# Performance work log

Measured on AMD Instinct MI355X. Metric: run time of the kernel, lower is better.

Reference implementation:

```python
import math
import jax
import jax.numpy as jnp
import numpy as np

N_IMG = 8
A = 3
H = 100
W = 100
STRIDE = 16
IMG = 1600
PRE_NMS_TOP_N = 2000
POST_NMS_TOP_N = 1000
NMS_THRESH = 0.7
MIN_SIZE = 0
BBOX_XFORM_CLIP = math.log(1000.0 / 16.0)


def setup_inputs() -> dict:
    key = jax.random.key(0)
    k1, k2 = jax.random.split(key)
    objectness = jax.random.normal(k1, (N_IMG, A, H, W), jnp.float32)
    box_regression = jax.random.normal(k2, (N_IMG, A * 4, H, W), jnp.float32) * 0.5
    # Grid anchors, flattened in (H, W, A) order to match objectness.permute(0,2,3,1)
    cy = (jnp.arange(H, dtype=jnp.float32) + 0.5) * STRIDE  # [H]
    cx = (jnp.arange(W, dtype=jnp.float32) + 0.5) * STRIDE  # [W]
    half = jnp.array([64.0, 128.0, 256.0], jnp.float32) / 2.0  # [A]
    cy = cy[:, None, None]  # [H,1,1]
    cx = cx[None, :, None]  # [1,W,1]
    s = half[None, None, :]  # [1,1,A]
    x1, y1, x2, y2 = jnp.broadcast_arrays(cx - s, cy - s, cx + s, cy + s)
    anc = jnp.stack([x1, y1, x2, y2], axis=-1).reshape(-1, 4)  # [H*W*A, 4]
    anchors = jnp.broadcast_to(anc[None], (N_IMG, H * W * A, 4)).copy()
    return {
        "objectness": objectness,
        "box_regression": box_regression,
        "anchors": anchors,
        "image_height": IMG,
        "image_width": IMG,
    }


def _decode(deltas, boxes):
    # BoxCoder(weights=(1,1,1,1)).decode with TO_REMOVE=1
    widths = boxes[..., 2] - boxes[..., 0] + 1.0
    heights = boxes[..., 3] - boxes[..., 1] + 1.0
    ctr_x = boxes[..., 0] + 0.5 * widths
    ctr_y = boxes[..., 1] + 0.5 * heights
    dx, dy = deltas[..., 0], deltas[..., 1]
    dw = jnp.minimum(deltas[..., 2], BBOX_XFORM_CLIP)
    dh = jnp.minimum(deltas[..., 3], BBOX_XFORM_CLIP)
    pcx = dx * widths + ctr_x
    pcy = dy * heights + ctr_y
    pw = jnp.exp(dw) * widths
    ph = jnp.exp(dh) * heights
    return jnp.stack(
        [pcx - 0.5 * pw, pcy - 0.5 * ph, pcx + 0.5 * pw - 1.0, pcy + 0.5 * ph - 1.0],
        axis=-1,
    )


def _nms_keep(boxes, valid, thresh):
    # boxes [n,4] sorted by descending score; valid: pre-filter mask.
    n = boxes.shape[0]
    x1, y1, x2, y2 = boxes[:, 0], boxes[:, 1], boxes[:, 2], boxes[:, 3]
    areas = (x2 - x1 + 1.0) * (y2 - y1 + 1.0)
    xx1 = jnp.maximum(x1[:, None], x1[None, :])
    yy1 = jnp.maximum(y1[:, None], y1[None, :])
    xx2 = jnp.minimum(x2[:, None], x2[None, :])
    yy2 = jnp.minimum(y2[:, None], y2[None, :])
    inter = jnp.maximum(xx2 - xx1 + 1.0, 0.0) * jnp.maximum(yy2 - yy1 + 1.0, 0.0)
    iou = inter / (areas[:, None] + areas[None, :] - inter)
    idx = jnp.arange(n)

    def body(i, keep):
        sup = keep[i] & (iou[i] > thresh) & (idx > i)
        return keep & ~sup

    return jax.lax.fori_loop(0, n, body, valid)


def _forward(objectness, box_regression, anchors, image_height, image_width):
    N, A_, H_, W_ = objectness.shape
    scores = jax.nn.sigmoid(objectness.transpose(0, 2, 3, 1).reshape(N, -1))  # [N, A*H*W]
    deltas = (
        box_regression.reshape(N, A_, 4, H_, W_)
        .transpose(0, 3, 4, 1, 2)
        .reshape(N, -1, 4)
    )
    pre = min(PRE_NMS_TOP_N, scores.shape[1])
    top_scores, top_idx = jax.lax.top_k(scores, pre)  # sorted descending
    deltas = jnp.take_along_axis(deltas, top_idx[:, :, None], axis=1)
    anc = jnp.take_along_axis(anchors, top_idx[:, :, None], axis=1)
    props = _decode(deltas, anc)  # [N, pre, 4]
    # clip to image (fact = 1)
    xs = jnp.clip(props[..., 0::2], 0.0, image_width - 1.0)
    ys = jnp.clip(props[..., 1::2], 0.0, image_height - 1.0)
    props = jnp.stack([xs[..., 0], ys[..., 0], xs[..., 1], ys[..., 1]], axis=-1)
    # filter small / out-of-image-center boxes
    ws = props[..., 2] - props[..., 0] + 1.0
    hs = props[..., 3] - props[..., 1] + 1.0
    xc = props[..., 0] + ws / 2.0
    yc = props[..., 1] + hs / 2.0
    valid = (ws >= MIN_SIZE) & (hs >= MIN_SIZE) & (xc < image_width) & (yc < image_height)
    keep = jax.vmap(lambda b, v: _nms_keep(b, v, NMS_THRESH))(props, valid)

    def _select(b, s, k):
        # compact kept boxes (already score-sorted) into fixed-size output
        rank = jnp.cumsum(k) - 1
        tgt = jnp.where(k & (rank < POST_NMS_TOP_N), rank, POST_NMS_TOP_N)
        ob = jnp.zeros((POST_NMS_TOP_N + 1, 4), b.dtype).at[tgt].set(b)[:POST_NMS_TOP_N]
        os = jnp.zeros((POST_NMS_TOP_N + 1,), s.dtype).at[tgt].set(s)[:POST_NMS_TOP_N]
        ov = jnp.arange(POST_NMS_TOP_N) < jnp.minimum(jnp.sum(k), POST_NMS_TOP_N)
        return ob, os, ov

    return jax.vmap(_select)(props, top_scores, keep)


def reference(objectness, box_regression, anchors, image_height, image_width):
    # Returns (boxes [N,post,4], objectness scores [N,post], valid mask [N,post])
    return _forward(objectness, box_regression, anchors, image_height, image_width)
```

## Files before the change

kernel.cpp:

```cpp
#include <hip/hip_runtime.h>
#include <math.h>
#include <stdint.h>

#define NIMG   8
#define NA     30000
#define PRE_N  2000
#define POST_N 1000
#define NMS_TH 0.7f
#define DCLIP  4.135166556742356f
#define IMGF   1600.0f
#define IMGM1  1599.0f
#define CAND_MAX 4096


__global__ __launch_bounds__(1024) void hist_compact(
    const float* __restrict__ obj,
    uint64_t* __restrict__ candBuf, unsigned int* __restrict__ candCnt)
{
    const int n    = blockIdx.x;
    const int tid  = threadIdx.x;
    const int lane = tid & 63;
    const int wid  = tid >> 6;

    __shared__ unsigned int hist[4096];
    __shared__ unsigned int wsum[16];
    __shared__ unsigned int scal[4];

    for (int b = tid; b < 4096; b += 1024) hist[b] = 0u;
    if (tid < 4) scal[tid] = 0u;
    __syncthreads();

    const float* objn = obj + n * NA;

    for (int j = tid; j < NA; j += 1024) {
        unsigned int u = __float_as_uint(objn[j]);
        unsigned int k = (u & 0x80000000u) ? ~u : (u | 0x80000000u);
        atomicAdd(&hist[k >> 20], 1u);
    }
    __syncthreads();

    unsigned int c0 = hist[tid*4+0], c1 = hist[tid*4+1],
                 c2 = hist[tid*4+2], c3 = hist[tid*4+3];
    unsigned int p = c0 + c1 + c2 + c3;
    unsigned int s = p;
    #pragma unroll
    for (int off = 1; off < 64; off <<= 1) {
        unsigned int v = __shfl_down(s, off);
        if (lane + off < 64) s += v;
    }
    if (lane == 0) wsum[wid] = s;
    __syncthreads();
    unsigned int wafter = 0;
    for (int w = wid + 1; w < 16; ++w) wafter += wsum[w];
    unsigned int after = (s - p) + wafter;
    {
        unsigned int S3 = after + c3;
        unsigned int S2 = S3 + c2;
        unsigned int S1 = S2 + c1;
        unsigned int S0 = S1 + c0;
        if (S3 >= PRE_N && after < PRE_N) { scal[2] = tid*4+3; }
        if (S2 >= PRE_N && S3    < PRE_N) { scal[2] = tid*4+2; }
        if (S1 >= PRE_N && S2    < PRE_N) { scal[2] = tid*4+1; }
        if (S0 >= PRE_N && S1    < PRE_N) { scal[2] = tid*4+0; }
    }
    __syncthreads();
    const unsigned int bstar = scal[2];

    for (int j = tid; j < NA; j += 1024) {
        unsigned int u = __float_as_uint(objn[j]);
        unsigned int k = (u & 0x80000000u) ? ~u : (u | 0x80000000u);
        if ((k >> 20) < bstar) continue;
        int a = j / 10000, t = j - a * 10000;
        uint64_t key = (((uint64_t)(~k)) << 32) | (unsigned int)(t * 3 + a);
        unsigned int pos = atomicAdd(&scal[0], 1u);
        if (pos < CAND_MAX) candBuf[n * CAND_MAX + pos] = key;
    }
    __syncthreads();
    if (tid == 0) candCnt[n] = min(scal[0], (unsigned int)CAND_MAX);
}

__global__ __launch_bounds__(64) void rank_decode(
    const float* __restrict__ breg,
    const uint64_t* __restrict__ candBuf, const unsigned int* __restrict__ candCnt,
    float* __restrict__ wsBoxes, float* __restrict__ wsScores,
    int* __restrict__ wsValid)
{
    const int n    = blockIdx.x >> 6;
    const int tile = blockIdx.x & 63;
    const int lane = threadIdx.x;

    const int C = (int)candCnt[n];
    if (tile * 64 >= C) return;

    const uint64_t* cb = candBuf + n * CAND_MAX;
    const int my = tile * 64 + lane;
    const uint64_t km = (my < C) ? cb[my] : ~0ull;

    unsigned int rank = 0;
    const int nch = (C + 63) >> 6;
    for (int ch = 0; ch < nch; ++ch) {
        const int j = ch * 64 + lane;
        uint64_t ck = (j < C) ? cb[j] : ~0ull;
        unsigned int clo = (unsigned int)ck, chi = (unsigned int)(ck >> 32);
        #pragma unroll
        for (int c = 0; c < 64; ++c) {
            unsigned int lo = (unsigned int)__builtin_amdgcn_readlane((int)clo, c);
            unsigned int hi = (unsigned int)__builtin_amdgcn_readlane((int)chi, c);
            uint64_t kc = ((uint64_t)hi << 32) | lo;
            rank += (kc < km) ? 1u : 0u;
        }
    }
    if (my >= C || rank >= PRE_N) return;

    unsigned int idx = (unsigned int)km;
    unsigned int k   = ~((unsigned int)(km >> 32));
    unsigned int u   = (k & 0x80000000u) ? (k & 0x7fffffffu) : ~k;
    float logit = __uint_as_float(u);
    float score = 1.0f / (1.0f + expf(-logit));

    int a = idx % 3, t = idx / 3, w = t % 100, h = t / 100;
    const float* bp = breg + n*120000 + (a*4)*10000 + t;
    float dx = bp[0], dy = bp[10000], dw = bp[20000], dh = bp[30000];

    float half = (a == 0) ? 32.0f : ((a == 1) ? 64.0f : 128.0f);
    float cx = w * 16.0f + 8.0f, cy = h * 16.0f + 8.0f;
    float x1 = cx - half, y1 = cy - half, x2 = cx + half, y2 = cy + half;
    float wd = x2 - x1 + 1.0f, hg = y2 - y1 + 1.0f;
    float cxr = x1 + 0.5f * wd, cyr = y1 + 0.5f * hg;
    dw = fminf(dw, DCLIP); dh = fminf(dh, DCLIP);
    float pcx = dx * wd + cxr, pcy = dy * hg + cyr;
    float pw = expf(dw) * wd, ph = expf(dh) * hg;
    float px1 = pcx - 0.5f * pw, py1 = pcy - 0.5f * ph;
    float px2 = pcx + 0.5f * pw - 1.0f, py2 = pcy + 0.5f * ph - 1.0f;
    px1 = fminf(fmaxf(px1, 0.0f), IMGM1);
    px2 = fminf(fmaxf(px2, 0.0f), IMGM1);
    py1 = fminf(fmaxf(py1, 0.0f), IMGM1);
    py2 = fminf(fmaxf(py2, 0.0f), IMGM1);
    float wss = px2 - px1 + 1.0f, hss = py2 - py1 + 1.0f;
    float xc = px1 + wss * 0.5f, yc = py1 + hss * 0.5f;
    int valid = (wss >= 0.0f) && (hss >= 0.0f) && (xc < IMGF) && (yc < IMGF);

    ((float4*)wsBoxes)[n * PRE_N + (int)rank] = make_float4(px1, py1, px2, py2);
    wsScores[n * PRE_N + (int)rank] = score;
    wsValid [n * PRE_N + (int)rank] = valid;
}

__global__ __launch_bounds__(512) void nms_mask(
    const float* __restrict__ wsBoxes, uint64_t* __restrict__ mask)
{
    const int blk  = blockIdx.x;
    const int n    = blk >> 5;
    const int i_t  = blk & 31;
    const int tid  = threadIdx.x;
    const int lane = tid & 63;
    const int wv   = tid >> 6;

    __shared__ uint64_t tile[64 * 33];

    for (int idx = tid; idx < 64 * 33; idx += 512) tile[idx] = 0ull;
    __syncthreads();

    const int r = i_t * 64 + lane;
    float4 rb = (r < PRE_N) ? ((const float4*)wsBoxes)[n * PRE_N + r]
                            : make_float4(0.f, 0.f, 0.f, 0.f);
    float ra = (rb.z - rb.x + 1.0f) * (rb.w - rb.y + 1.0f);

    for (int j_t = i_t + wv; j_t < 32; j_t += 8) {
        const int j = j_t * 64 + lane;
        float4 cb = (j < PRE_N) ? ((const float4*)wsBoxes)[n * PRE_N + j]
                                : make_float4(3e30f, 3e30f, 3e30f, 3e30f);
        float ca = (cb.z - cb.x + 1.0f) * (cb.w - cb.y + 1.0f);
        const uint64_t jmask = (j_t == 31) ? 0xFFFFull : ~0ull;
        const bool diag = (j_t == i_t);
        uint64_t myword = 0ull;

        #pragma unroll
        for (int c = 0; c < 64; ++c) {
            float rx1 = __int_as_float(__builtin_amdgcn_readlane(__float_as_int(rb.x), c));
            float ry1 = __int_as_float(__builtin_amdgcn_readlane(__float_as_int(rb.y), c));
            float rx2 = __int_as_float(__builtin_amdgcn_readlane(__float_as_int(rb.z), c));
            float ry2 = __int_as_float(__builtin_amdgcn_readlane(__float_as_int(rb.w), c));
            float rar = __int_as_float(__builtin_amdgcn_readlane(__float_as_int(ra), c));
            float xx1 = fmaxf(rx1, cb.x), yy1 = fmaxf(ry1, cb.y);
            float xx2 = fminf(rx2, cb.z), yy2 = fminf(ry2, cb.w);
            float ww = fmaxf(xx2 - xx1 + 1.0f, 0.0f);
            float hh = fmaxf(yy2 - yy1 + 1.0f, 0.0f);
            float inter = ww * hh;
            float denom = rar + ca - inter;
            unsigned long long bits = __ballot(inter > NMS_TH * denom) & jmask;
            if (diag) bits &= (c == 63) ? 0ull : ((~0ull) << (c + 1));
            if (lane == c) myword = bits;
        }
        tile[lane * 33 + j_t] = myword;
    }
    __syncthreads();

    uint64_t* mrow = mask + ((size_t)n * PRE_N + (size_t)i_t * 64) * 32;
    const int cmax = (i_t == 31) ? 16 : 64;
    for (int idx = tid; idx < cmax * 32; idx += 512) {
        const int rr = idx >> 5, w = idx & 31;
        mrow[idx] = tile[rr * 33 + w];
    }
}

#define SL(n,b) \
    "global_load_dword v" #n ", %[voff], %[sbase]\n\t" \
    "v_add_u32 %[voff], 0x100, %[voff]\n\t"

#define SS(n,b) \
    "s_waitcnt vmcnt(63)\n\t" \
    "v_readlane_b32 %[t], v" #n ", %[lw]\n\t" \
    "s_bitcmp1_b32 %[win], " #b "\n\t" \
    "s_cselect_b32 %[m], 0, -1\n\t" \
    "s_sub_i32 %[kept], %[kept], %[m]\n\t" \
    "s_and_b32 %[t], %[t], %[m]\n\t" \
    "s_or_b32 %[win], %[win], %[t]\n\t" \
    "v_and_b32 v" #n ", %[m], v" #n "\n\t" \
    "v_or_b32 %[rem], %[rem], v" #n "\n\t" \
    "global_load_dword v" #n ", %[voff], %[sbase]\n\t" \
    "v_add_u32 %[voff], 0x100, %[voff]\n\t"

#define SN(n,b,w) \
    "s_waitcnt vmcnt(" #w ")\n\t" \
    "v_readlane_b32 %[t], v" #n ", %[lw]\n\t" \
    "s_bitcmp1_b32 %[win], " #b "\n\t" \
    "s_cselect_b32 %[m], 0, -1\n\t" \
    "s_sub_i32 %[kept], %[kept], %[m]\n\t" \
    "s_and_b32 %[t], %[t], %[m]\n\t" \
    "s_or_b32 %[win], %[win], %[t]\n\t" \
    "v_and_b32 v" #n ", %[m], v" #n "\n\t" \
    "v_or_b32 %[rem], %[rem], v" #n "\n\t"

#define SWIN \
    "s_add_u32 %[lw], %[lw], 1\n\t" \
    "v_readlane_b32 %[t], %[rem], %[lw]\n\t" \
    "s_mov_b32 %[win], %[t]\n\t"

#define ROW_A(M) M(64,0) M(65,1) M(66,2) M(67,3) M(68,4) M(69,5) M(70,6) M(71,7) \
    M(72,8) M(73,9) M(74,10) M(75,11) M(76,12) M(77,13) M(78,14) M(79,15) \
    M(80,16) M(81,17) M(82,18) M(83,19) M(84,20) M(85,21) M(86,22) M(87,23) \
    M(88,24) M(89,25) M(90,26) M(91,27) M(92,28) M(93,29) M(94,30) M(95,31)
#define ROW_B(M) M(96,0) M(97,1) M(98,2) M(99,3) M(100,4) M(101,5) M(102,6) M(103,7) \
    M(104,8) M(105,9) M(106,10) M(107,11) M(108,12) M(109,13) M(110,14) M(111,15) \
    M(112,16) M(113,17) M(114,18) M(115,19) M(116,20) M(117,21) M(118,22) M(119,23) \
    M(120,24) M(121,25) M(122,26) M(123,27) M(124,28) M(125,29) M(126,30) M(127,31)

__global__ __launch_bounds__(256) void nms_scan_select(
    const float* __restrict__ wsBoxes, const float* __restrict__ wsScores,
    const int* __restrict__ wsValid, const uint64_t* __restrict__ mask,
    float* __restrict__ out)
{
    const int n   = blockIdx.x;
    const int tid = threadIdx.x;

    __shared__ __align__(8) unsigned char invb[256];
    __shared__ unsigned int keepw32[64];
    __shared__ int sscan[256];

    unsigned int byte = 0xFFu;
    if (tid < PRE_N / 8) {
        byte = 0u;
        for (int q = 0; q < 8; ++q)
            byte |= (wsValid[n * PRE_N + tid * 8 + q] ? 0u : 1u) << q;
    }
    invb[tid] = (unsigned char)byte;
    __syncthreads();

    if (tid < 64) {
        unsigned int rem = ((const unsigned int*)invb)[tid];
        unsigned long long sbase =
            (unsigned long long)(const void*)(mask + (size_t)n * PRE_N * 32);
        unsigned int voff = (unsigned int)(tid * 4);
        int win_, m_, t_, lw_, kept_, cnt_;

        asm volatile(
            "s_waitcnt vmcnt(0) lgkmcnt(0)\n\t"
            "s_mov_b32 %[kept], 0\n\t"
            "s_mov_b32 %[lw], 0\n\t"
            ROW_A(SL) ROW_B(SL)
            "v_readlane_b32 %[t], %[rem], %[lw]\n\t"
            "s_mov_b32 %[win], %[t]\n\t"
            "s_mov_b32 %[cnt], 30\n\t"
            "Lnms_%=:\n\t"
            ROW_A(SS)
            SWIN
            ROW_B(SS)
            SWIN
            "s_cmp_ge_i32 %[kept], 0x3e8\n\t"
            "s_cbranch_scc1 Lend_%=\n\t"
            "s_sub_u32 %[cnt], %[cnt], 1\n\t"
            "s_cmp_lg_u32 %[cnt], 0\n\t"
            "s_cbranch_scc1 Lnms_%=\n\t"
            SS(64,0) SS(65,1) SS(66,2) SS(67,3) SS(68,4) SS(69,5) SS(70,6) SS(71,7)
            SS(72,8) SS(73,9) SS(74,10) SS(75,11) SS(76,12) SS(77,13) SS(78,14) SS(79,15)
            SN(80,16,63) SN(81,17,62) SN(82,18,61) SN(83,19,60)
            SN(84,20,59) SN(85,21,58) SN(86,22,57) SN(87,23,56)
            SN(88,24,55) SN(89,25,54) SN(90,26,53) SN(91,27,52)
            SN(92,28,51) SN(93,29,50) SN(94,30,49) SN(95,31,48)
            SWIN
            SN(96,0,47) SN(97,1,46) SN(98,2,45) SN(99,3,44)
            SN(100,4,43) SN(101,5,42) SN(102,6,41) SN(103,7,40)
            SN(104,8,39) SN(105,9,38) SN(106,10,37) SN(107,11,36)
            SN(108,12,35) SN(109,13,34) SN(110,14,33) SN(111,15,32)
            SN(112,16,31) SN(113,17,30) SN(114,18,29) SN(115,19,28)
            SN(116,20,27) SN(117,21,26) SN(118,22,25) SN(119,23,24)
            SN(120,24,23) SN(121,25,22) SN(122,26,21) SN(123,27,20)
            SN(124,28,19) SN(125,29,18) SN(126,30,17) SN(127,31,16)
            SWIN
            SN(64,0,15) SN(65,1,14) SN(66,2,13) SN(67,3,12)
            SN(68,4,11) SN(69,5,10) SN(70,6,9) SN(71,7,8)
            SN(72,8,7) SN(73,9,6) SN(74,10,5) SN(75,11,4)
            SN(76,12,3) SN(77,13,2) SN(78,14,1) SN(79,15,0)
            "Lend_%=:\n\t"
            "s_waitcnt vmcnt(0)\n\t"
            : [rem]"+v"(rem), [voff]"+v"(voff),
              [win]"=&s"(win_), [m]"=&s"(m_), [t]"=&s"(t_),
              [lw]"=&s"(lw_), [kept]"=&s"(kept_), [cnt]"=&s"(cnt_)
            : [sbase]"s"(sbase)
            : "scc", "vcc", "memory",
              "v64","v65","v66","v67","v68","v69","v70","v71",
              "v72","v73","v74","v75","v76","v77","v78","v79",
              "v80","v81","v82","v83","v84","v85","v86","v87",
              "v88","v89","v90","v91","v92","v93","v94","v95",
              "v96","v97","v98","v99","v100","v101","v102","v103",
              "v104","v105","v106","v107","v108","v109","v110","v111",
              "v112","v113","v114","v115","v116","v117","v118","v119",
              "v120","v121","v122","v123","v124","v125","v126","v127");

        keepw32[tid] = ~rem;
    }
    __syncthreads();

    int c[8]; const int base8 = tid * 8;
    int lsum = 0;
    for (int q = 0; q < 8; ++q) {
        const int i = base8 + q;
        c[q] = (i < PRE_N) ? (int)((keepw32[i >> 5] >> (i & 31)) & 1u) : 0;
        lsum += c[q];
    }
    sscan[tid] = lsum;
    __syncthreads();
    for (int off = 1; off < 256; off <<= 1) {
        int v = (tid >= off) ? sscan[tid - off] : 0;
        __syncthreads();
        sscan[tid] += v;
        __syncthreads();
    }
    const int excl  = sscan[tid] - lsum;
    const int total = sscan[255];

    float* ob  = out + n * POST_N * 4;
    float* osc = out + NIMG * POST_N * 4 + n * POST_N;
    float* ovd = out + NIMG * POST_N * 5 + n * POST_N;

    for (int i = tid; i < POST_N * 4; i += 256) ob[i] = 0.0f;
    for (int i = tid; i < POST_N; i += 256) osc[i] = 0.0f;
    const int lim = min(total, POST_N);
    for (int i = tid; i < POST_N; i += 256) ovd[i] = (i < lim) ? 1.0f : 0.0f;
    __syncthreads();

    int run = excl;
    for (int q = 0; q < 8; ++q) {
        const int i = base8 + q;
        if (i < PRE_N && c[q]) {
            if (run < POST_N) {
                float4 b = ((const float4*)wsBoxes)[n * PRE_N + i];
                ob[run * 4 + 0] = b.x;
                ob[run * 4 + 1] = b.y;
                ob[run * 4 + 2] = b.z;
                ob[run * 4 + 3] = b.w;
                osc[run] = wsScores[n * PRE_N + i];
            }
            run++;
        }
    }
}

extern "C" void kernel_launch(void* const* d_in, const int* in_sizes, int n_in,
                              void* d_out, int out_size, void* d_ws, size_t ws_size,
                              hipStream_t stream) {
    const float* obj  = (const float*)d_in[0];
    const float* breg = (const float*)d_in[1];
    float* ws        = (float*)d_ws;
    float* wsBoxes   = ws;
    float* wsScores  = ws + 64000;
    int*   wsValid   = (int*)(ws + 80000);
    uint64_t* wsMask = (uint64_t*)(ws + 96000);
    uint64_t*     candBuf = wsMask;
    unsigned int* candCnt = (unsigned int*)(wsMask + NIMG * CAND_MAX);

    hist_compact<<<NIMG, 1024, 0, stream>>>(obj, candBuf, candCnt);
    rank_decode<<<NIMG * 64, 64, 0, stream>>>(breg, candBuf, candCnt,
                                              wsBoxes, wsScores, wsValid);
    nms_mask<<<NIMG * 32, 512, 0, stream>>>(wsBoxes, wsMask);
    nms_scan_select<<<NIMG, 256, 0, stream>>>(wsBoxes, wsScores, wsValid, wsMask,
                                              (float*)d_out);
}
```

Baseline: 184.1 us.

## Fuse NMS mask and scan kernels via last-block-done atomic counter

New measurement: 190.9 us. 1.04x slower.

```diff
diff --git a/kernel.cpp b/kernel.cpp
--- a/kernel.cpp
+++ b/kernel.cpp
@@ -15,7 +15,8 @@
 
 __global__ __launch_bounds__(1024) void hist_compact(
     const float* __restrict__ obj,
-    uint64_t* __restrict__ candBuf, unsigned int* __restrict__ candCnt)
+    uint64_t* __restrict__ candBuf, unsigned int* __restrict__ candCnt,
+    unsigned int* __restrict__ doneArr)
 {
     const int n    = blockIdx.x;
     const int tid  = threadIdx.x;
@@ -28,6 +29,7 @@
 
     for (int b = tid; b < 4096; b += 1024) hist[b] = 0u;
     if (tid < 4) scal[tid] = 0u;
+    if (tid == 0) doneArr[n] = 0u;
     __syncthreads();
 
     const float* objn = obj + n * NA;
@@ -145,8 +147,52 @@
     wsValid [n * PRE_N + (int)rank] = valid;
 }
 
-__global__ __launch_bounds__(512) void nms_mask(
-    const float* __restrict__ wsBoxes, uint64_t* __restrict__ mask)
+#define SL(n,b) \
+    "global_load_dword v" #n ", %[voff], %[sbase]\n\t" \
+    "v_add_u32 %[voff], 0x100, %[voff]\n\t"
+
+#define SS(n,b) \
+    "s_waitcnt vmcnt(63)\n\t" \
+    "v_readlane_b32 %[t], v" #n ", %[lw]\n\t" \
+    "s_bitcmp1_b32 %[win], " #b "\n\t" \
+    "s_cselect_b32 %[m], 0, -1\n\t" \
+    "s_sub_i32 %[kept], %[kept], %[m]\n\t" \
+    "s_and_b32 %[t], %[t], %[m]\n\t" \
+    "s_or_b32 %[win], %[win], %[t]\n\t" \
+    "v_and_b32 v" #n ", %[m], v" #n "\n\t" \
+    "v_or_b32 %[rem], %[rem], v" #n "\n\t" \
+    "global_load_dword v" #n ", %[voff], %[sbase]\n\t" \
+    "v_add_u32 %[voff], 0x100, %[voff]\n\t"
+
+#define SN(n,b,w) \
+    "s_waitcnt vmcnt(" #w ")\n\t" \
+    "v_readlane_b32 %[t], v" #n ", %[lw]\n\t" \
+    "s_bitcmp1_b32 %[win], " #b "\n\t" \
+    "s_cselect_b32 %[m], 0, -1\n\t" \
+    "s_sub_i32 %[kept], %[kept], %[m]\n\t" \
+    "s_and_b32 %[t], %[t], %[m]\n\t" \
+    "s_or_b32 %[win], %[win], %[t]\n\t" \
+    "v_and_b32 v" #n ", %[m], v" #n "\n\t" \
+    "v_or_b32 %[rem], %[rem], v" #n "\n\t"
+
+#define SWIN \
+    "s_add_u32 %[lw], %[lw], 1\n\t" \
+    "v_readlane_b32 %[t], %[rem], %[lw]\n\t" \
+    "s_mov_b32 %[win], %[t]\n\t"
+
+#define ROW_A(M) M(64,0) M(65,1) M(66,2) M(67,3) M(68,4) M(69,5) M(70,6) M(71,7) \
+    M(72,8) M(73,9) M(74,10) M(75,11) M(76,12) M(77,13) M(78,14) M(79,15) \
+    M(80,16) M(81,17) M(82,18) M(83,19) M(84,20) M(85,21) M(86,22) M(87,23) \
+    M(88,24) M(89,25) M(90,26) M(91,27) M(92,28) M(93,29) M(94,30) M(95,31)
+#define ROW_B(M) M(96,0) M(97,1) M(98,2) M(99,3) M(100,4) M(101,5) M(102,6) M(103,7) \
+    M(104,8) M(105,9) M(106,10) M(107,11) M(108,12) M(109,13) M(110,14) M(111,15) \
+    M(112,16) M(113,17) M(114,18) M(115,19) M(116,20) M(117,21) M(118,22) M(119,23) \
+    M(120,24) M(121,25) M(122,26) M(123,27) M(124,28) M(125,29) M(126,30) M(127,31)
+
+__global__ __launch_bounds__(512) void nms_mask_scan(
+    const float* __restrict__ wsBoxes, const float* __restrict__ wsScores,
+    const int* __restrict__ wsValid, uint64_t* __restrict__ mask,
+    unsigned int* __restrict__ doneArr, float* __restrict__ out)
 {
     const int blk  = blockIdx.x;
     const int n    = blk >> 5;
@@ -156,6 +202,10 @@
     const int wv   = tid >> 6;
 
     __shared__ uint64_t tile[64 * 33];
+    __shared__ int sScan[512];
+    __shared__ __align__(8) unsigned char sInvb[256];
+    __shared__ unsigned int sKeep[64];
+    __shared__ unsigned int sFlag;
 
     for (int idx = tid; idx < 64 * 33; idx += 512) tile[idx] = 0ull;
     __syncthreads();
@@ -201,73 +251,29 @@
         const int rr = idx >> 5, w = idx & 31;
         mrow[idx] = tile[rr * 33 + w];
     }
-}
-
-#define SL(n,b) \
-    "global_load_dword v" #n ", %[voff], %[sbase]\n\t" \
-    "v_add_u32 %[voff], 0x100, %[voff]\n\t"
-
-#define SS(n,b) \
-    "s_waitcnt vmcnt(63)\n\t" \
-    "v_readlane_b32 %[t], v" #n ", %[lw]\n\t" \
-    "s_bitcmp1_b32 %[win], " #b "\n\t" \
-    "s_cselect_b32 %[m], 0, -1\n\t" \
-    "s_sub_i32 %[kept], %[kept], %[m]\n\t" \
-    "s_and_b32 %[t], %[t], %[m]\n\t" \
-    "s_or_b32 %[win], %[win], %[t]\n\t" \
-    "v_and_b32 v" #n ", %[m], v" #n "\n\t" \
-    "v_or_b32 %[rem], %[rem], v" #n "\n\t" \
-    "global_load_dword v" #n ", %[voff], %[sbase]\n\t" \
-    "v_add_u32 %[voff], 0x100, %[voff]\n\t"
-
-#define SN(n,b,w) \
-    "s_waitcnt vmcnt(" #w ")\n\t" \
-    "v_readlane_b32 %[t], v" #n ", %[lw]\n\t" \
-    "s_bitcmp1_b32 %[win], " #b "\n\t" \
-    "s_cselect_b32 %[m], 0, -1\n\t" \
-    "s_sub_i32 %[kept], %[kept], %[m]\n\t" \
-    "s_and_b32 %[t], %[t], %[m]\n\t" \
-    "s_or_b32 %[win], %[win], %[t]\n\t" \
-    "v_and_b32 v" #n ", %[m], v" #n "\n\t" \
-    "v_or_b32 %[rem], %[rem], v" #n "\n\t"
-
-#define SWIN \
-    "s_add_u32 %[lw], %[lw], 1\n\t" \
-    "v_readlane_b32 %[t], %[rem], %[lw]\n\t" \
-    "s_mov_b32 %[win], %[t]\n\t"
-
-#define ROW_A(M) M(64,0) M(65,1) M(66,2) M(67,3) M(68,4) M(69,5) M(70,6) M(71,7) \
-    M(72,8) M(73,9) M(74,10) M(75,11) M(76,12) M(77,13) M(78,14) M(79,15) \
-    M(80,16) M(81,17) M(82,18) M(83,19) M(84,20) M(85,21) M(86,22) M(87,23) \
-    M(88,24) M(89,25) M(90,26) M(91,27) M(92,28) M(93,29) M(94,30) M(95,31)
-#define ROW_B(M) M(96,0) M(97,1) M(98,2) M(99,3) M(100,4) M(101,5) M(102,6) M(103,7) \
-    M(104,8) M(105,9) M(106,10) M(107,11) M(108,12) M(109,13) M(110,14) M(111,15) \
-    M(112,16) M(113,17) M(114,18) M(115,19) M(116,20) M(117,21) M(118,22) M(119,23) \
-    M(120,24) M(121,25) M(122,26) M(123,27) M(124,28) M(125,29) M(126,30) M(127,31)
-
-__global__ __launch_bounds__(256) void nms_scan_select(
-    const float* __restrict__ wsBoxes, const float* __restrict__ wsScores,
-    const int* __restrict__ wsValid, const uint64_t* __restrict__ mask,
-    float* __restrict__ out)
-{
-    const int n   = blockIdx.x;
-    const int tid = threadIdx.x;
-
-    __shared__ __align__(8) unsigned char invb[256];
-    __shared__ unsigned int keepw32[64];
-    __shared__ int sscan[256];
-
-    unsigned int byte = 0xFFu;
-    if (tid < PRE_N / 8) {
-        byte = 0u;
-        for (int q = 0; q < 8; ++q)
-            byte |= (wsValid[n * PRE_N + tid * 8 + q] ? 0u : 1u) << q;
-    }
-    invb[tid] = (unsigned char)byte;
+    __syncthreads();
+
+    if (tid == 0) {
+        __threadfence();
+        sFlag = atomicAdd(&doneArr[n], 1u);
+    }
+    __syncthreads();
+    if (sFlag != 31u) return;
+    __threadfence();
+
+    if (tid < 256) {
+        unsigned int byte = 0xFFu;
+        if (tid < PRE_N / 8) {
+            byte = 0u;
+            for (int q = 0; q < 8; ++q)
+                byte |= (wsValid[n * PRE_N + tid * 8 + q] ? 0u : 1u) << q;
+        }
+        sInvb[tid] = (unsigned char)byte;
+    }
     __syncthreads();
 
     if (tid < 64) {
-        unsigned int rem = ((const unsigned int*)invb)[tid];
+        unsigned int rem = ((const unsigned int*)sInvb)[tid];
         unsigned long long sbase =
             (unsigned long long)(const void*)(mask + (size_t)n * PRE_N * 32);
         unsigned int voff = (unsigned int)(tid * 4);
@@ -327,42 +333,42 @@
               "v112","v113","v114","v115","v116","v117","v118","v119",
               "v120","v121","v122","v123","v124","v125","v126","v127");
 
-        keepw32[tid] = ~rem;
-    }
-    __syncthreads();
-
-    int c[8]; const int base8 = tid * 8;
+        sKeep[tid] = ~rem;
+    }
+    __syncthreads();
+
+    int cf[4]; const int base4 = tid * 4;
     int lsum = 0;
-    for (int q = 0; q < 8; ++q) {
-        const int i = base8 + q;
-        c[q] = (i < PRE_N) ? (int)((keepw32[i >> 5] >> (i & 31)) & 1u) : 0;
-        lsum += c[q];
-    }
-    sscan[tid] = lsum;
-    __syncthreads();
-    for (int off = 1; off < 256; off <<= 1) {
-        int v = (tid >= off) ? sscan[tid - off] : 0;
+    for (int q = 0; q < 4; ++q) {
+        const int i = base4 + q;
+        cf[q] = (i < PRE_N) ? (int)((sKeep[i >> 5] >> (i & 31)) & 1u) : 0;
+        lsum += cf[q];
+    }
+    sScan[tid] = lsum;
+    __syncthreads();
+    for (int off = 1; off < 512; off <<= 1) {
+        int v = (tid >= off) ? sScan[tid - off] : 0;
         __syncthreads();
-        sscan[tid] += v;
+        sScan[tid] += v;
         __syncthreads();
     }
-    const int excl  = sscan[tid] - lsum;
-    const int total = sscan[255];
+    const int excl  = sScan[tid] - lsum;
+    const int total = sScan[511];
 
     float* ob  = out + n * POST_N * 4;
     float* osc = out + NIMG * POST_N * 4 + n * POST_N;
     float* ovd = out + NIMG * POST_N * 5 + n * POST_N;
 
-    for (int i = tid; i < POST_N * 4; i += 256) ob[i] = 0.0f;
-    for (int i = tid; i < POST_N; i += 256) osc[i] = 0.0f;
+    for (int i = tid; i < POST_N * 4; i += 512) ob[i] = 0.0f;
+    for (int i = tid; i < POST_N; i += 512) osc[i] = 0.0f;
     const int lim = min(total, POST_N);
-    for (int i = tid; i < POST_N; i += 256) ovd[i] = (i < lim) ? 1.0f : 0.0f;
+    for (int i = tid; i < POST_N; i += 512) ovd[i] = (i < lim) ? 1.0f : 0.0f;
     __syncthreads();
 
     int run = excl;
-    for (int q = 0; q < 8; ++q) {
-        const int i = base8 + q;
-        if (i < PRE_N && c[q]) {
+    for (int q = 0; q < 4; ++q) {
+        const int i = base4 + q;
+        if (i < PRE_N && cf[q]) {
             if (run < POST_N) {
                 float4 b = ((const float4*)wsBoxes)[n * PRE_N + i];
                 ob[run * 4 + 0] = b.x;
@@ -388,11 +394,12 @@
     uint64_t* wsMask = (uint64_t*)(ws + 96000);
     uint64_t*     candBuf = wsMask;
     unsigned int* candCnt = (unsigned int*)(wsMask + NIMG * CAND_MAX);
-
-    hist_compact<<<NIMG, 1024, 0, stream>>>(obj, candBuf, candCnt);
+    unsigned int* doneArr =
+        (unsigned int*)((char*)wsMask + (size_t)NIMG * PRE_N * 32 * 8);
+
+    hist_compact<<<NIMG, 1024, 0, stream>>>(obj, candBuf, candCnt, doneArr);
     rank_decode<<<NIMG * 64, 64, 0, stream>>>(breg, candBuf, candCnt,
                                               wsBoxes, wsScores, wsValid);
-    nms_mask<<<NIMG * 32, 512, 0, stream>>>(wsBoxes, wsMask);
-    nms_scan_select<<<NIMG, 256, 0, stream>>>(wsBoxes, wsScores, wsValid, wsMask,
-                                              (float*)d_out);
+    nms_mask_scan<<<NIMG * 32, 512, 0, stream>>>(wsBoxes, wsScores, wsValid,
+                                                 wsMask, doneArr, (float*)d_out);
 }
```
